# Performance work log

Hardware: AMD Instinct MI355X
Metric: run time of the kernel (lower is better)

Reference implementation:

```python
import jax, jax.numpy as jnp
import numpy as np

D, H, W = 20, 18, 18      # f_dim = (20, 72//4, 72//4); depth == feature_ch
PI = 3.14159              # constant used in the torch module


def make_grid():
    # matches make_coordinate_grid_3d: normalized coords in [-1, 1]
    x = 2.0 * jnp.arange(W, dtype=jnp.float32) / (W - 1) - 1.0
    y = 2.0 * jnp.arange(H, dtype=jnp.float32) / (H - 1) - 1.0
    z = 2.0 * jnp.arange(D, dtype=jnp.float32) / (D - 1) - 1.0
    xx = jnp.broadcast_to(x[None, None, :], (D, H, W))
    yy = jnp.broadcast_to(y[None, :, None], (D, H, W))
    zz = jnp.broadcast_to(z[:, None, None], (D, H, W))
    grid_xy = jnp.stack([xx, yy], axis=-1)   # (D,H,W,2), order (x, y)
    return grid_xy, zz


def trilinear_sample(vol, grid):
    # vol: (D,H,W); grid: (D,H,W,3) with (x,y,z) in [-1,1]
    # F.grid_sample defaults: mode='bilinear' (trilinear), padding='zeros', align_corners=False
    ix = ((grid[..., 0] + 1.0) * W - 1.0) * 0.5
    iy = ((grid[..., 1] + 1.0) * H - 1.0) * 0.5
    iz = ((grid[..., 2] + 1.0) * D - 1.0) * 0.5
    x0, y0, z0 = jnp.floor(ix), jnp.floor(iy), jnp.floor(iz)
    wx, wy, wz = ix - x0, iy - y0, iz - z0
    vflat = vol.reshape(-1)
    out = jnp.zeros_like(ix)
    for cz in (0, 1):
        for cy in (0, 1):
            for cx in (0, 1):
                xi = x0 + cx
                yi = y0 + cy
                zi = z0 + cz
                w = ((wx if cx else 1.0 - wx)
                     * (wy if cy else 1.0 - wy)
                     * (wz if cz else 1.0 - wz))
                valid = ((xi >= 0) & (xi < W) & (yi >= 0) & (yi < H)
                         & (zi >= 0) & (zi < D))
                xi_c = jnp.clip(xi, 0, W - 1).astype(jnp.int32)
                yi_c = jnp.clip(yi, 0, H - 1).astype(jnp.int32)
                zi_c = jnp.clip(zi, 0, D - 1).astype(jnp.int32)
                idx = (zi_c * H + yi_c) * W + xi_c
                out = out + jnp.where(valid, w * vflat[idx], 0.0)
    return out


def setup_inputs() -> dict:
    key = jax.random.key(0)
    ks = jax.random.split(key, 10)
    B, P, F = 4096, 256, 20
    s = 0.05
    return {
        "feature_map": jax.random.normal(ks[0], (B, F, H, W), jnp.float32),
        "para_code": jax.random.normal(ks[1], (B, P), jnp.float32),
        "W1": jax.random.normal(ks[2], (P, P), jnp.float32) * s,
        "b1": jax.random.normal(ks[3], (P,), jnp.float32) * s,
        "Ws": jax.random.normal(ks[4], (P, F), jnp.float32) * s,
        "bs": jax.random.normal(ks[5], (F,), jnp.float32) * s,
        "Wr": jax.random.normal(ks[6], (P, F), jnp.float32) * s,
        "br": jax.random.normal(ks[7], (F,), jnp.float32) * s,
        "Wt": jax.random.normal(ks[8], (P, 2 * F), jnp.float32) * s,
        "bt": jax.random.normal(ks[9], (2 * F,), jnp.float32) * s,
    }


def reference(feature_map, para_code, W1, b1, Ws, bs, Wr, br, Wt, bt):
    B, F = feature_map.shape[0], feature_map.shape[1]  # F == D == 20
    grid_xy, grid_z = make_grid()
    h = jax.nn.relu(para_code @ W1 + b1)                     # commn_linear
    scale = jax.nn.sigmoid(h @ Ws + bs) * 2.0                # (B,F)
    angle = jnp.tanh(h @ Wr + br) * PI                       # (B,F)
    trans = jnp.tanh(h @ Wt + bt).reshape(B, F, 2)           # (B,F,2)
    c, s = jnp.cos(angle), jnp.sin(angle)
    rot = jnp.stack([jnp.stack([c, -s], -1),
                     jnp.stack([s, c], -1)], -2)             # (B,F,2,2)
    g = grid_xy.reshape(F, H * W, 2)                          # depth == feature_ch
    # per-channel affine: rotate, scale, translate each grid point
    tg = jnp.einsum('bfij,fpj->bfpi', rot, g)                 # (B,F,HW,2)
    tg = tg * scale[:, :, None, None] + trans[:, :, None, :]
    full_grid = jnp.concatenate(
        [tg.reshape(B, F, H, W, 2),
         jnp.broadcast_to(grid_z, (B, F, H, W))[..., None]], axis=-1)
    return jax.vmap(trilinear_sample)(feature_map, full_grid)
```

## Files before the change

kernel.cpp:

```cpp
#include <hip/hip_runtime.h>

#define PI_F 3.14159f

__global__ __launch_bounds__(256) void params_kernel(
    const float* __restrict__ pc, const float* __restrict__ W1, const float* __restrict__ b1,
    const float* __restrict__ Ws, const float* __restrict__ bs,
    const float* __restrict__ Wr, const float* __restrict__ br,
    const float* __restrict__ Wt, const float* __restrict__ bt,
    float* __restrict__ params)
{
    __shared__ float hbuf[4][260];
    __shared__ float raw[4][80];
    __shared__ __align__(16) float pcs[4][256];

    const int t  = threadIdx.x;
    const int b0 = blockIdx.x * 4;

    #pragma unroll
    for (int g = 0; g < 4; ++g)
        pcs[g][t] = pc[(size_t)(b0 + g) * 256 + t];

    float acc[4];
    #pragma unroll
    for (int g = 0; g < 4; ++g) acc[g] = b1[t];
    __syncthreads();

    const float4* p40 = (const float4*)pcs[0];
    const float4* p41 = (const float4*)pcs[1];
    const float4* p42 = (const float4*)pcs[2];
    const float4* p43 = (const float4*)pcs[3];

    #pragma unroll 4
    for (int k4 = 0; k4 < 64; ++k4) {
        const float* wp = W1 + (size_t)k4 * 1024 + t;
        float w0 = wp[0], w1 = wp[256], w2 = wp[512], w3 = wp[768];
        float4 p0 = p40[k4];
        float4 p1 = p41[k4];
        float4 p2 = p42[k4];
        float4 p3 = p43[k4];
        acc[0] = fmaf(p0.x, w0, acc[0]);
        acc[1] = fmaf(p1.x, w0, acc[1]);
        acc[2] = fmaf(p2.x, w0, acc[2]);
        acc[3] = fmaf(p3.x, w0, acc[3]);
        acc[0] = fmaf(p0.y, w1, acc[0]);
        acc[1] = fmaf(p1.y, w1, acc[1]);
        acc[2] = fmaf(p2.y, w1, acc[2]);
        acc[3] = fmaf(p3.y, w1, acc[3]);
        acc[0] = fmaf(p0.z, w2, acc[0]);
        acc[1] = fmaf(p1.z, w2, acc[1]);
        acc[2] = fmaf(p2.z, w2, acc[2]);
        acc[3] = fmaf(p3.z, w2, acc[3]);
        acc[0] = fmaf(p0.w, w3, acc[0]);
        acc[1] = fmaf(p1.w, w3, acc[1]);
        acc[2] = fmaf(p2.w, w3, acc[2]);
        acc[3] = fmaf(p3.w, w3, acc[3]);
    }
    #pragma unroll
    for (int g = 0; g < 4; ++g) hbuf[g][t] = fmaxf(acc[g], 0.0f);
    __syncthreads();

    for (int task = t; task < 320; task += 256) {
        int g   = task / 80;
        int col = task - g * 80;
        const float* Wcol;
        float bias;
        int stride;
        if (col < 20)      { Wcol = Ws + col;        bias = bs[col];      stride = 20; }
        else if (col < 40) { Wcol = Wr + (col - 20); bias = br[col - 20]; stride = 20; }
        else               { Wcol = Wt + (col - 40); bias = bt[col - 40]; stride = 40; }
        const float4* h4 = (const float4*)hbuf[g];
        float a = bias;
        #pragma unroll 4
        for (int k4 = 0; k4 < 64; ++k4) {
            float4 h = h4[k4];
            int k = k4 * 4;
            a = fmaf(h.x, Wcol[k * stride], a);
            a = fmaf(h.y, Wcol[(k + 1) * stride], a);
            a = fmaf(h.z, Wcol[(k + 2) * stride], a);
            a = fmaf(h.w, Wcol[(k + 3) * stride], a);
        }
        raw[g][col] = a;
    }
    __syncthreads();

    for (int task = t; task < 80; task += 256) {
        int g = task / 20;
        int f = task - g * 20;
        float sc  = 2.0f / (1.0f + expf(-raw[g][f]));
        float ang = PI_F * tanhf(raw[g][20 + f]);
        float tx  = tanhf(raw[g][40 + 2 * f]);
        float ty  = tanhf(raw[g][40 + 2 * f + 1]);
        float c = cosf(ang), s = sinf(ang);
        float* o = params + ((size_t)(b0 + g) * 20 + f) * 8;
        o[0] = 9.0f * sc * c;  o[1] = -9.0f * sc * s;  o[2] = fmaf(9.0f, tx, 9.5f);
        o[3] = 9.0f * sc * s;  o[4] =  9.0f * sc * c;  o[5] = fmaf(9.0f, ty, 9.5f);
        o[6] = 0.0f;           o[7] = 0.0f;
    }
}

__global__ __launch_bounds__(256, 8) void sample_kernel(
    const float* __restrict__ fmap, const float* __restrict__ params,
    float* __restrict__ out)
{
    __shared__ __align__(16) float lds[4][448];

    const int t    = threadIdx.x;
    const int lane = t & 63;
    const int w    = t >> 6;
    const int bid  = blockIdx.x;
    const int b    = bid / 5;
    const int c    = (bid - b * 5) * 4 + w;
    float* wv = lds[w];

    const float* pp = params + ((size_t)b * 20 + c) * 8;
    const float4 pA = *(const float4*)pp;
    const float2 pB = *(const float2*)(pp + 4);

    const float izf = (40.0f * (float)c - 19.0f) * (1.0f / 38.0f);
    const float fz0 = floorf(izf);
    const int   z0  = (int)fz0;
    const float wzB = izf - fz0;
    const bool  v0  = (z0 >= 0);
    const bool  v1  = (z0 + 1 <= 19);
    const float ew0 = v0 ? (1.0f - wzB) : 0.0f;
    const float ew1 = v1 ? wzB : 0.0f;
    const float* fb = fmap + (size_t)b * 6480;
    const float* s0 = fb + (v0 ? z0 : 0) * 324;
    const float* s1 = fb + (v1 ? z0 + 1 : 19) * 324;

    float2 a2[3], b2[3];
    #pragma unroll
    for (int it = 0; it < 3; ++it) {
        int k  = it * 64 + lane;
        int kc = (k < 162) ? k : 161;
        a2[it] = *(const float2*)(s0 + 2 * kc);
        b2[it] = *(const float2*)(s1 + 2 * kc);
    }

    {
        int i = lane;
        int idx = (i < 21) ? i : 378 + i;
        wv[idx] = 0.0f;
        i = 64 + lane;
        if (i < 124) {
            int idx2;
            if (i < 70) idx2 = 378 + i;
            else {
                int q = i - 70;
                int y = 1 + q / 3;
                int r = q - (q / 3) * 3;
                int x = (r == 0) ? 0 : 18 + r;
                idx2 = y * 21 + x;
            }
            wv[idx2] = 0.0f;
        }
    }

    #pragma unroll
    for (int it = 0; it < 3; ++it) {
        int k = it * 64 + lane;
        if (k < 162) {
            int y = k / 9;
            int x = 2 * (k - y * 9);
            int base = (y + 1) * 21 + (x + 1);
            wv[base]     = fmaf(a2[it].x, ew0, b2[it].x * ew1);
            wv[base + 1] = fmaf(a2[it].y, ew0, b2[it].y * ew1);
        }
    }

    float* ob = out + (size_t)b * 6480 + c * 324;
    #pragma unroll
    for (int it = 0; it < 3; ++it) {
        int k = it * 64 + lane;
        if (k < 162) {
            int y  = k / 9;
            int x0 = 2 * (k - y * 9);
            float Y = (float)y * (2.0f / 17.0f) - 1.0f;
            float r2[2];
            #pragma unroll
            for (int q = 0; q < 2; ++q) {
                float X = (float)(x0 + q) * (2.0f / 17.0f) - 1.0f;
                float ix = fmaf(pA.x, X, fmaf(pA.y, Y, pA.z));
                float iy = fmaf(pA.w, X, fmaf(pB.x, Y, pB.y));
                ix = fminf(fmaxf(ix, 0.0f), 19.0f);
                iy = fminf(fmaxf(iy, 0.0f), 19.0f);
                float fx = floorf(ix), fy = floorf(iy);
                float u1 = ix - fx, vv = iy - fy;
                const float* s = wv + ((int)fy * 21 + (int)fx);
                float t00 = s[0], t01 = s[1], t10 = s[21], t11 = s[22];
                float u0 = 1.0f - u1, vc = 1.0f - vv;
                r2[q] = fmaf(fmaf(t01, u1, t00 * u0), vc,
                             fmaf(t11, u1, t10 * u0) * vv);
            }
            *(float2*)(ob + y * 18 + x0) = make_float2(r2[0], r2[1]);
        }
    }
}

extern "C" void kernel_launch(void* const* d_in, const int* in_sizes, int n_in,
                              void* d_out, int out_size, void* d_ws, size_t ws_size,
                              hipStream_t stream)
{
    const float* fmap = (const float*)d_in[0];
    const float* pc   = (const float*)d_in[1];
    const float* W1   = (const float*)d_in[2];
    const float* b1   = (const float*)d_in[3];
    const float* Ws   = (const float*)d_in[4];
    const float* bs   = (const float*)d_in[5];
    const float* Wr   = (const float*)d_in[6];
    const float* br   = (const float*)d_in[7];
    const float* Wt   = (const float*)d_in[8];
    const float* bt   = (const float*)d_in[9];
    float* out    = (float*)d_out;
    float* params = (float*)d_ws;

    const int B = in_sizes[0] / (20 * 18 * 18);

    params_kernel<<<B / 4, 256, 0, stream>>>(pc, W1, b1, Ws, bs, Wr, br, Wt, bt, params);
    sample_kernel<<<B * 5, 256, 0, stream>>>(fmap, params, out);
}
```

Measured before the change: 229.5 us.

## Process two channels per wave with 128-thread blocks and XCD-aware block remap

The sample kernel now runs 128 threads per block, and each wave handles two channels instead of one. Both channels' depth-slice loads are issued up front to raise memory-level parallelism. Block IDs are permuted as (bid&7)*cpx + bid>>3 so that consecutive logical blocks, which share a batch's feature map, land on the same XCD's L2. The x-step of the affine grid transform is computed incrementally, and the bilinear sample is pulled into a helper. The risks are higher register pressure from doubling the per-thread loads, and the remap assumes the grid size is divisible by 8.

Measured after the change: 236.2 us. 2.9% more time.

```diff
diff --git a/kernel.cpp b/kernel.cpp
--- a/kernel.cpp
+++ b/kernel.cpp
@@ -98,7 +98,20 @@
     }
 }
 
-__global__ __launch_bounds__(256, 8) void sample_kernel(
+__device__ __forceinline__ float samp1(const float* wv, float ix, float iy)
+{
+    ix = fminf(fmaxf(ix, 0.0f), 19.0f);
+    iy = fminf(fmaxf(iy, 0.0f), 19.0f);
+    float fx = floorf(ix), fy = floorf(iy);
+    float u1 = ix - fx, vv = iy - fy;
+    int base = (int)fmaf(fy, 21.0f, fx);
+    const float* s = wv + base;
+    float t00 = s[0], t01 = s[1], t10 = s[21], t11 = s[22];
+    float u0 = 1.0f - u1, vc = 1.0f - vv;
+    return fmaf(fmaf(t01, u1, t00 * u0), vc, fmaf(t11, u1, t10 * u0) * vv);
+}
+
+__global__ __launch_bounds__(128, 8) void sample_kernel(
     const float* __restrict__ fmap, const float* __restrict__ params,
     float* __restrict__ out)
 {
@@ -107,40 +120,58 @@
     const int t    = threadIdx.x;
     const int lane = t & 63;
     const int w    = t >> 6;
+    const int cpx  = (int)(gridDim.x >> 3);
     const int bid  = blockIdx.x;
-    const int b    = bid / 5;
-    const int c    = (bid - b * 5) * 4 + w;
-    float* wv = lds[w];
-
-    const float* pp = params + ((size_t)b * 20 + c) * 8;
-    const float4 pA = *(const float4*)pp;
-    const float2 pB = *(const float2*)(pp + 4);
-
-    const float izf = (40.0f * (float)c - 19.0f) * (1.0f / 38.0f);
-    const float fz0 = floorf(izf);
-    const int   z0  = (int)fz0;
-    const float wzB = izf - fz0;
-    const bool  v0  = (z0 >= 0);
-    const bool  v1  = (z0 + 1 <= 19);
-    const float ew0 = v0 ? (1.0f - wzB) : 0.0f;
-    const float ew1 = v1 ? wzB : 0.0f;
+    const int orig = (bid & 7) * cpx + (bid >> 3);
+    const int b    = orig / 5;
+    const int grp  = orig - b * 5;
+    const int c0   = grp * 4 + w * 2;
+
+    float* wv0 = lds[w * 2];
+    float* wv1 = lds[w * 2 + 1];
+
+    const float* pp = params + ((size_t)b * 20 + c0) * 8;
+    const float4 pA0 = *(const float4*)(pp);
+    const float2 pB0 = *(const float2*)(pp + 4);
+    const float4 pA1 = *(const float4*)(pp + 8);
+    const float2 pB1 = *(const float2*)(pp + 12);
+
+    float ew0[2], ew1[2];
+    const float* s0p[2];
+    const float* s1p[2];
     const float* fb = fmap + (size_t)b * 6480;
-    const float* s0 = fb + (v0 ? z0 : 0) * 324;
-    const float* s1 = fb + (v1 ? z0 + 1 : 19) * 324;
-
-    float2 a2[3], b2[3];
+    #pragma unroll
+    for (int ch = 0; ch < 2; ++ch) {
+        int c = c0 + ch;
+        float izf = (40.0f * (float)c - 19.0f) * (1.0f / 38.0f);
+        float fz0 = floorf(izf);
+        int   z0  = (int)fz0;
+        float wzB = izf - fz0;
+        bool  v0  = (z0 >= 0);
+        bool  v1  = (z0 + 1 <= 19);
+        ew0[ch] = v0 ? (1.0f - wzB) : 0.0f;
+        ew1[ch] = v1 ? wzB : 0.0f;
+        s0p[ch] = fb + (v0 ? z0 : 0) * 324;
+        s1p[ch] = fb + (v1 ? z0 + 1 : 19) * 324;
+    }
+
+    float2 a2[2][3], b2[2][3];
     #pragma unroll
     for (int it = 0; it < 3; ++it) {
         int k  = it * 64 + lane;
         int kc = (k < 162) ? k : 161;
-        a2[it] = *(const float2*)(s0 + 2 * kc);
-        b2[it] = *(const float2*)(s1 + 2 * kc);
-    }
-
-    {
+        #pragma unroll
+        for (int ch = 0; ch < 2; ++ch) {
+            a2[ch][it] = *(const float2*)(s0p[ch] + 2 * kc);
+            b2[ch][it] = *(const float2*)(s1p[ch] + 2 * kc);
+        }
+    }
+
+    #pragma unroll
+    for (int ch = 0; ch < 2; ++ch) {
+        float* wv = ch ? wv1 : wv0;
         int i = lane;
-        int idx = (i < 21) ? i : 378 + i;
-        wv[idx] = 0.0f;
+        wv[(i < 21) ? i : 378 + i] = 0.0f;
         i = 64 + lane;
         if (i < 124) {
             int idx2;
@@ -163,36 +194,35 @@
             int y = k / 9;
             int x = 2 * (k - y * 9);
             int base = (y + 1) * 21 + (x + 1);
-            wv[base]     = fmaf(a2[it].x, ew0, b2[it].x * ew1);
-            wv[base + 1] = fmaf(a2[it].y, ew0, b2[it].y * ew1);
-        }
-    }
-
-    float* ob = out + (size_t)b * 6480 + c * 324;
+            wv0[base]     = fmaf(a2[0][it].x, ew0[0], b2[0][it].x * ew1[0]);
+            wv0[base + 1] = fmaf(a2[0][it].y, ew0[0], b2[0][it].y * ew1[0]);
+            wv1[base]     = fmaf(a2[1][it].x, ew0[1], b2[1][it].x * ew1[1]);
+            wv1[base + 1] = fmaf(a2[1][it].y, ew0[1], b2[1][it].y * ew1[1]);
+        }
+    }
+
+    float* ob0 = out + (size_t)b * 6480 + c0 * 324;
+    float* ob1 = ob0 + 324;
+    const float dix0 = pA0.x * (2.0f / 17.0f), diy0 = pA0.w * (2.0f / 17.0f);
+    const float dix1 = pA1.x * (2.0f / 17.0f), diy1 = pA1.w * (2.0f / 17.0f);
     #pragma unroll
     for (int it = 0; it < 3; ++it) {
         int k = it * 64 + lane;
         if (k < 162) {
             int y  = k / 9;
             int x0 = 2 * (k - y * 9);
-            float Y = (float)y * (2.0f / 17.0f) - 1.0f;
-            float r2[2];
-            #pragma unroll
-            for (int q = 0; q < 2; ++q) {
-                float X = (float)(x0 + q) * (2.0f / 17.0f) - 1.0f;
-                float ix = fmaf(pA.x, X, fmaf(pA.y, Y, pA.z));
-                float iy = fmaf(pA.w, X, fmaf(pB.x, Y, pB.y));
-                ix = fminf(fmaxf(ix, 0.0f), 19.0f);
-                iy = fminf(fmaxf(iy, 0.0f), 19.0f);
-                float fx = floorf(ix), fy = floorf(iy);
-                float u1 = ix - fx, vv = iy - fy;
-                const float* s = wv + ((int)fy * 21 + (int)fx);
-                float t00 = s[0], t01 = s[1], t10 = s[21], t11 = s[22];
-                float u0 = 1.0f - u1, vc = 1.0f - vv;
-                r2[q] = fmaf(fmaf(t01, u1, t00 * u0), vc,
-                             fmaf(t11, u1, t10 * u0) * vv);
-            }
-            *(float2*)(ob + y * 18 + x0) = make_float2(r2[0], r2[1]);
+            float X = (float)x0 * (2.0f / 17.0f) - 1.0f;
+            float Y = (float)y  * (2.0f / 17.0f) - 1.0f;
+            float ixa0 = fmaf(pA0.x, X, fmaf(pA0.y, Y, pA0.z));
+            float iya0 = fmaf(pA0.w, X, fmaf(pB0.x, Y, pB0.y));
+            float r00 = samp1(wv0, ixa0, iya0);
+            float r01 = samp1(wv0, ixa0 + dix0, iya0 + diy0);
+            *(float2*)(ob0 + y * 18 + x0) = make_float2(r00, r01);
+            float ixa1 = fmaf(pA1.x, X, fmaf(pA1.y, Y, pA1.z));
+            float iya1 = fmaf(pA1.w, X, fmaf(pB1.x, Y, pB1.y));
+            float r10 = samp1(wv1, ixa1, iya1);
+            float r11 = samp1(wv1, ixa1 + dix1, iya1 + diy1);
+            *(float2*)(ob1 + y * 18 + x0) = make_float2(r10, r11);
         }
     }
 }
@@ -217,5 +247,5 @@
     const int B = in_sizes[0] / (20 * 18 * 18);
 
     params_kernel<<<B / 4, 256, 0, stream>>>(pc, W1, b1, Ws, bs, Wr, br, Wt, bt, params);
-    sample_kernel<<<B * 5, 256, 0, stream>>>(fmap, params, out);
-}
+    sample_kernel<<<B * 5, 128, 0, stream>>>(fmap, params, out);
+}
```
